# Optimization experiments

Hardware: AMD Instinct MI355X
Metric: run time of the kernel (lower is better)

## Reference

```python
import jax, jax.numpy as jnp
import numpy as np

WIDTH = 2048
NUM_HEADS = 16
HEAD_DIM = WIDTH // NUM_HEADS
WINDOW = 1024
B, T = 4, 2048
MIN_LOGIT = -2.3819763e+38
MAX_WAVELENGTH = 10000.0


def apply_rope(x, positions):
    # x: [b, t, n, h]; RoPE on first half of h, pass-through second half
    b, t, n, h = x.shape
    x_rope, x_pass = jnp.split(x, 2, axis=-1)
    half = x_rope.shape[-1] // 2
    freq_exponents = 2.0 * jnp.arange(half, dtype=jnp.float32) / (2 * half)
    inv_freq = MAX_WAVELENGTH ** (-freq_exponents)  # [half]
    sinusoid = positions.astype(jnp.float32).reshape(1, t, 1, 1) * inv_freq  # [1,t,1,half]
    sin = jnp.sin(sinusoid).astype(x.dtype)
    cos = jnp.cos(sinusoid).astype(x.dtype)
    x1, x2 = jnp.split(x_rope, 2, axis=-1)
    return jnp.concatenate([x1 * cos - x2 * sin, x2 * cos + x1 * sin, x_pass], axis=-1)


def setup_inputs() -> dict:
    key = jax.random.key(0)
    ks = jax.random.split(key, 6)
    x = jax.random.normal(ks[0], (B, T, WIDTH), dtype=jnp.float32)
    segment_pos = jnp.arange(T, dtype=jnp.int32)
    # forward-pass mask: single segment, causal + window
    pos = jnp.arange(T)
    attention_mask = (pos[:, None] >= pos[None, :]) & (pos[:, None] <= pos[None, :] + WINDOW)
    std = np.sqrt(1.0 / WIDTH)
    wq = jax.random.normal(ks[1], (WIDTH, WIDTH), dtype=jnp.float32) * std
    wk = jax.random.normal(ks[2], (HEAD_DIM, WIDTH), dtype=jnp.float32) * std
    wv = jax.random.normal(ks[3], (HEAD_DIM, WIDTH), dtype=jnp.float32) * std
    w_out = jax.random.normal(ks[4], (WIDTH, WIDTH), dtype=jnp.float32) * std
    b_out = jnp.zeros((WIDTH,), dtype=jnp.float32)
    return {"x": x, "segment_pos": segment_pos, "attention_mask": attention_mask,
            "wq": wq, "wk": wk, "wv": wv, "w_out": w_out, "b_out": b_out}


def reference(x, segment_pos, attention_mask, wq, wk, wv, w_out, b_out):
    b, t, _ = x.shape
    q = (x @ wq.T).reshape(b, t, NUM_HEADS, HEAD_DIM)  # [b,t,n,h]
    k = (x @ wk.T).reshape(b, t, 1, HEAD_DIM)          # single shared KV head (MQA)
    v = x @ wv.T                                        # [b,t,h]
    q = apply_rope(q, segment_pos)
    k = apply_rope(k, segment_pos)[:, :, 0]             # [b,t,h]
    logits = jnp.einsum('btnh,bsh->bnts', q, k).astype(jnp.float32) * (HEAD_DIM ** -0.5)
    logits = jnp.where(attention_mask[None, None], logits, MIN_LOGIT)
    probs = jax.nn.softmax(logits, axis=-1).astype(x.dtype)
    encoded = jnp.einsum('bnts,bsh->btnh', probs, v).reshape(b, t, WIDTH)
    return encoded @ w_out.T + b_out
```

## Files before the change

kernel.cpp:

```cpp
#include <hip/hip_runtime.h>
#include <stdint.h>


#define WIDTH_ 2048
#define NHEADS_ 16
#define HD_ 128
#define WINDOW_ 1024
#define B_ 4
#define T_ 2048
#define MROWS_ (B_ * T_)
#define NQKV_ (WIDTH_ + 2 * HD_)

typedef float f32x4 __attribute__((ext_vector_type(4)));
typedef __bf16 bf16x8 __attribute__((ext_vector_type(8)));
typedef float f32x4v __attribute__((ext_vector_type(4)));
typedef unsigned short u16;
typedef unsigned int u32;

__device__ __forceinline__ u16 f2bf(float x) {
  u32 u = __builtin_bit_cast(u32, x);
  return (u16)((u + 0x7FFFu + ((u >> 16) & 1u)) >> 16);
}
__device__ __forceinline__ float bf2f(u16 b) {
  u32 u = ((u32)b) << 16;
  return __builtin_bit_cast(float, u);
}
__device__ __forceinline__ u32 pack2bf(float a, float b) {
  union { __bf16 h[2]; u32 u; } c;
  c.h[0] = (__bf16)a; c.h[1] = (__bf16)b;
  return c.u;
}

__device__ __forceinline__ f32x4 mfma16(bf16x8 a, bf16x8 b, f32x4 c) {
  return __builtin_amdgcn_mfma_f32_16x16x32_bf16(a, b, c, 0, 0, 0);
}

#define GLL16(gp, lp)                                          \
  __builtin_amdgcn_global_load_lds(                            \
      (const __attribute__((address_space(1))) void*)(gp),     \
      (__attribute__((address_space(3))) void*)(lp), 16, 0, 0)

__global__ __launch_bounds__(256) void cvt_f32_bf16(const float* __restrict__ src,
                                                    u16* __restrict__ dst, int n4) {
  int i = blockIdx.x * blockDim.x + threadIdx.x;
  int stride = gridDim.x * blockDim.x;
  for (; i < n4; i += stride) {
    f32x4v v = *reinterpret_cast<const f32x4v*>(src + 4 * (size_t)i);
    u32 lo = (u32)f2bf(v[0]) | ((u32)f2bf(v[1]) << 16);
    u32 hi = (u32)f2bf(v[2]) | ((u32)f2bf(v[3]) << 16);
    uint2 o;
    o.x = lo; o.y = hi;
    *reinterpret_cast<uint2*>(dst + 4 * (size_t)i) = o;
  }
}

__global__ __launch_bounds__(256) void cvt_weights(const float* __restrict__ wq,
                                                   const float* __restrict__ wk,
                                                   const float* __restrict__ wv,
                                                   const float* __restrict__ wo,
                                                   u16* __restrict__ wqkv,
                                                   u16* __restrict__ wob) {
  const int NQ = WIDTH_ * WIDTH_ / 4;
  const int NK = HD_ * WIDTH_ / 4;
  const int NO = WIDTH_ * WIDTH_ / 4;
  const int total = NQ + 2 * NK + NO;
  int i = blockIdx.x * blockDim.x + threadIdx.x;
  int stride = gridDim.x * blockDim.x;
  for (; i < total; i += stride) {
    const float* s;
    u16* d;
    int j;
    if (i < NQ) { s = wq; d = wqkv; j = i; }
    else if (i < NQ + NK) { s = wk; d = wqkv + (size_t)WIDTH_ * WIDTH_; j = i - NQ; }
    else if (i < NQ + 2 * NK) { s = wv; d = wqkv + (size_t)(WIDTH_ + HD_) * WIDTH_; j = i - NQ - NK; }
    else { s = wo; d = wob; j = i - NQ - 2 * NK; }
    f32x4v v = *reinterpret_cast<const f32x4v*>(s + 4 * (size_t)j);
    uint2 o;
    o.x = (u32)f2bf(v[0]) | ((u32)f2bf(v[1]) << 16);
    o.y = (u32)f2bf(v[2]) | ((u32)f2bf(v[3]) << 16);
    *reinterpret_cast<uint2*>(d + 4 * (size_t)j) = o;
  }
}

template <bool F32OUT>
__global__ __launch_bounds__(256) void gemm_bt(const u16* __restrict__ A,
                                               const u16* __restrict__ W,
                                               void* __restrict__ Cout,
                                               const float* __restrict__ bias,
                                               int M, int N, int K) {
  __shared__ alignas(16) u16 As[128 * 32];
  __shared__ alignas(16) u16 Bs[128 * 32];
  const int tid = threadIdx.x;
  const int wid = tid >> 6, lane = tid & 63;
  const int g = lane >> 4, lr = lane & 15;
  const int m0 = blockIdx.y << 7, n0 = blockIdx.x << 7;
  const int wm = wid >> 1, wn = wid & 1;

  const f32x4 vzero = {0.f, 0.f, 0.f, 0.f};
  f32x4 acc[4][4];
#pragma unroll
  for (int i = 0; i < 4; i++)
#pragma unroll
    for (int j = 0; j < 4; j++) acc[i][j] = vzero;

  const int c0 = wid * 2, c1 = wid * 2 + 1;
  const int lrow = lane >> 2;
  const int lcol = (lane & 3) * 8;
  const u16* a0 = A + (size_t)(m0 + c0 * 16 + lrow) * K + lcol;
  const u16* a1 = A + (size_t)(m0 + c1 * 16 + lrow) * K + lcol;
  const u16* b0 = W + (size_t)(n0 + c0 * 16 + lrow) * K + lcol;
  const u16* b1 = W + (size_t)(n0 + c1 * 16 + lrow) * K + lcol;

  for (int k0 = 0; k0 < K; k0 += 32) {
    __syncthreads();
    GLL16(a0 + k0, &As[c0 * 512]);
    GLL16(a1 + k0, &As[c1 * 512]);
    GLL16(b0 + k0, &Bs[c0 * 512]);
    GLL16(b1 + k0, &Bs[c1 * 512]);
    __syncthreads();

    bf16x8 af[4], bfv[4];
#pragma unroll
    for (int mi = 0; mi < 4; mi++)
      af[mi] = *(const bf16x8*)&As[(wm * 64 + mi * 16 + lr) * 32 + g * 8];
#pragma unroll
    for (int ni = 0; ni < 4; ni++)
      bfv[ni] = *(const bf16x8*)&Bs[(wn * 64 + ni * 16 + lr) * 32 + g * 8];
#pragma unroll
    for (int mi = 0; mi < 4; mi++)
#pragma unroll
      for (int ni = 0; ni < 4; ni++)
        acc[mi][ni] = mfma16(af[mi], bfv[ni], acc[mi][ni]);
  }

#pragma unroll
  for (int mi = 0; mi < 4; mi++) {
    int row = m0 + wm * 64 + mi * 16 + g * 4;
#pragma unroll
    for (int ni = 0; ni < 4; ni++) {
      int col = n0 + wn * 64 + ni * 16 + lr;
#pragma unroll
      for (int r = 0; r < 4; r++) {
        float v = acc[mi][ni][r];
        if (F32OUT) {
          ((float*)Cout)[(size_t)(row + r) * N + col] = v + bias[col];
        } else {
          ((u16*)Cout)[(size_t)(row + r) * N + col] = f2bf(v);
        }
      }
    }
  }
}

template <bool F32OUT>
__global__ __launch_bounds__(512, 2) void gemm256(const u16* __restrict__ A,
                                                  const u16* __restrict__ W,
                                                  void* __restrict__ Cout,
                                                  const float* __restrict__ bias,
                                                  int M, int N, int K) {
  __shared__ alignas(16) u16 As[3][256 * 32];
  __shared__ alignas(16) u16 Bs[3][256 * 32];
  const int tid = threadIdx.x;
  const int wid = tid >> 6, lane = tid & 63;
  const int g = lane >> 4, lr = lane & 15;
  const int wm = wid >> 2, wn = wid & 3;

  const int nwg = gridDim.x;
  const int o = blockIdx.x;
  const int wg = (o & 7) * (nwg >> 3) + (o >> 3);
  const int NT = N >> 8;
  const int mt = wg / NT, nt = wg % NT;
  const int m0 = mt << 8, n0 = nt << 8;

  const u16* pa[2];
  const u16* pb[2];
#pragma unroll
  for (int j = 0; j < 2; j++) {
    int row = wid * 32 + j * 16 + (lane >> 2);
    int sc = (lane & 3) ^ ((row >> 1) & 3);
    pa[j] = A + (size_t)(m0 + row) * K + sc * 8;
    pb[j] = W + (size_t)(n0 + row) * K + sc * 8;
  }
  const int ldsoff = wid * 2048;

  const f32x4 vzero = {0.f, 0.f, 0.f, 0.f};
  f32x4 acc[8][4];
#pragma unroll
  for (int i = 0; i < 8; i++)
#pragma unroll
    for (int j = 0; j < 4; j++) acc[i][j] = vzero;

#define STAGE_A(bi, k0)                                        \
  do {                                                         \
    GLL16(pa[0] + (k0), (char*)As[bi] + ldsoff);               \
    GLL16(pa[1] + (k0), (char*)As[bi] + ldsoff + 1024);        \
  } while (0)
#define STAGE_B(bi, k0)                                        \
  do {                                                         \
    GLL16(pb[0] + (k0), (char*)Bs[bi] + ldsoff);               \
    GLL16(pb[1] + (k0), (char*)Bs[bi] + ldsoff + 1024);        \
  } while (0)

  STAGE_A(0, 0); STAGE_B(0, 0);
  STAGE_A(1, 32); STAGE_B(1, 32);
  asm volatile("s_waitcnt vmcnt(4)" ::: "memory");
  __builtin_amdgcn_sched_barrier(0);
  __builtin_amdgcn_s_barrier();

  const int ntk = K >> 5;
  int cur = 0;
  for (int t = 0; t < ntk; ++t) {
    const int nx2 = (cur + 2 >= 3) ? cur - 1 : cur + 2;
    const char* aB = (const char*)As[cur];
    const char* bB = (const char*)Bs[cur];
    const bool pre = (t + 2 < ntk);

    bf16x8 bfv[4], af[4];
#pragma unroll
    for (int ni = 0; ni < 4; ni++) {
      int row = wn * 64 + ni * 16 + lr;
      bfv[ni] = *(const bf16x8*)(bB + row * 64 + ((g ^ ((row >> 1) & 3)) << 4));
    }
#pragma unroll
    for (int mi = 0; mi < 4; mi++) {
      int row = wm * 128 + mi * 16 + lr;
      af[mi] = *(const bf16x8*)(aB + row * 64 + ((g ^ ((row >> 1) & 3)) << 4));
    }
    if (pre) STAGE_A(nx2, (t + 2) << 5);
    __builtin_amdgcn_s_barrier();
    asm volatile("s_waitcnt lgkmcnt(0)" ::: "memory");
    __builtin_amdgcn_sched_barrier(0);
    __builtin_amdgcn_s_setprio(1);
#pragma unroll
    for (int mi = 0; mi < 4; mi++)
#pragma unroll
      for (int ni = 0; ni < 4; ni++)
        acc[mi][ni] = mfma16(af[mi], bfv[ni], acc[mi][ni]);
    __builtin_amdgcn_s_setprio(0);
    __builtin_amdgcn_s_barrier();

    bf16x8 af2[4];
#pragma unroll
    for (int mi = 0; mi < 4; mi++) {
      int row = wm * 128 + 64 + mi * 16 + lr;
      af2[mi] = *(const bf16x8*)(aB + row * 64 + ((g ^ ((row >> 1) & 3)) << 4));
    }
    if (pre) STAGE_B(nx2, (t + 2) << 5);
    __builtin_amdgcn_s_barrier();
    asm volatile("s_waitcnt lgkmcnt(0)" ::: "memory");
    __builtin_amdgcn_sched_barrier(0);
    __builtin_amdgcn_s_setprio(1);
#pragma unroll
    for (int mi = 0; mi < 4; mi++)
#pragma unroll
      for (int ni = 0; ni < 4; ni++)
        acc[mi + 4][ni] = mfma16(af2[mi], bfv[ni], acc[mi + 4][ni]);
    __builtin_amdgcn_s_setprio(0);

    if (pre) {
      asm volatile("s_waitcnt vmcnt(4)" ::: "memory");
    } else if (t + 1 < ntk) {
      asm volatile("s_waitcnt vmcnt(0)" ::: "memory");
    }
    __builtin_amdgcn_sched_barrier(0);
    __builtin_amdgcn_s_barrier();

    cur = (cur + 1 >= 3) ? 0 : cur + 1;
  }
#undef STAGE_A
#undef STAGE_B

#pragma unroll
  for (int mi = 0; mi < 8; mi++) {
    int row = m0 + wm * 128 + mi * 16 + g * 4;
#pragma unroll
    for (int ni = 0; ni < 4; ni++) {
      int col = n0 + wn * 64 + ni * 16 + lr;
#pragma unroll
      for (int r = 0; r < 4; r++) {
        float v = acc[mi][ni][r];
        if (F32OUT) {
          ((float*)Cout)[(size_t)(row + r) * N + col] = v + bias[col];
        } else {
          ((u16*)Cout)[(size_t)(row + r) * N + col] = f2bf(v);
        }
      }
    }
  }
}

__global__ __launch_bounds__(256) void rope_scatter(const u16* __restrict__ Qraw,
                                                    const u16* __restrict__ KVraw,
                                                    const int* __restrict__ segpos,
                                                    u16* __restrict__ Qb,
                                                    u16* __restrict__ Kb,
                                                    u16* __restrict__ VT) {
  const int row = blockIdx.x;
  const int b = row / T_, t = row % T_;
  const float pos = (float)segpos[t];
  const u16* qsrc = Qraw + (size_t)row * WIDTH_;
  const u16* kvsrc = KVraw + (size_t)row * 256;
  const int tid = threadIdx.x;
  const float L2_10K_OVER_32 = 0.4152410118609203f;

  for (int j = tid; j < NHEADS_ * 32; j += 256) {
    int h = j >> 5, d = j & 31;
    float inv = exp2f(-(float)d * L2_10K_OVER_32);
    float ang = pos * inv;
    float sn = sinf(ang), cs = cosf(ang);
    int c1 = h * HD_ + d, c2 = c1 + 32;
    float x1 = bf2f(qsrc[c1]), x2 = bf2f(qsrc[c2]);
    Qb[(size_t)row * WIDTH_ + c1] = f2bf(x1 * cs - x2 * sn);
    Qb[(size_t)row * WIDTH_ + c2] = f2bf(x2 * cs + x1 * sn);
  }
  for (int j = tid; j < NHEADS_ * 64; j += 256) {
    int h = j >> 6, d = j & 63;
    int c = h * HD_ + 64 + d;
    Qb[(size_t)row * WIDTH_ + c] = qsrc[c];
  }
  if (tid < 32) {
    int d = tid;
    float inv = exp2f(-(float)d * L2_10K_OVER_32);
    float ang = pos * inv;
    float sn = sinf(ang), cs = cosf(ang);
    float x1 = bf2f(kvsrc[d]), x2 = bf2f(kvsrc[d + 32]);
    Kb[(size_t)row * HD_ + d] = f2bf(x1 * cs - x2 * sn);
    Kb[(size_t)row * HD_ + d + 32] = f2bf(x2 * cs + x1 * sn);
  } else if (tid >= 64 && tid < 128) {
    int d = tid;
    Kb[(size_t)row * HD_ + d] = kvsrc[d];
  }
  for (int j = tid; j < HD_; j += 256) {
    VT[((size_t)b * HD_ + j) * T_ + t] = kvsrc[HD_ + j];
  }
}

__global__ __launch_bounds__(256, 2) void attn(const u16* __restrict__ Qb,
                                               const u16* __restrict__ Kb,
                                               const u16* __restrict__ VT,
                                               u16* __restrict__ Eb) {
  __shared__ alignas(16) u16 Ks[2][64 * 128];
  __shared__ alignas(16) u16 Vs[2][128 * 64];
  __shared__ alignas(16) u16 Ps[4][2][16 * 64];

  const int tid = threadIdx.x;
  const int wid = tid >> 6, lane = tid & 63;
  const int g = lane >> 4, lr = lane & 15;
  const int nqt = T_ / 128;
  const int qt = blockIdx.x % nqt;
  const int n = (blockIdx.x / nqt) % NHEADS_;
  const int b = blockIdx.x / (nqt * NHEADS_);
  const int q0b = qt * 128;
  const int q0w = q0b + wid * 32;

  const char* kptr = (const char*)(Kb + (size_t)b * T_ * HD_);
  const char* vptr = (const char*)(VT + (size_t)b * HD_ * T_);

  const char* srcb[8];
  int smul;
  if (wid < 2) {
    smul = HD_ * 2;
#pragma unroll
    for (int i = 0; i < 8; i++) {
      int row = wid * 32 + i * 4 + (lane >> 4);
      int c = (lane & 15) << 4;
      srcb[i] = kptr + (size_t)row * 256 + (c ^ ((row & 7) << 4));
    }
  } else {
    smul = 2;
#pragma unroll
    for (int i = 0; i < 8; i++) {
      int row = (wid - 2) * 64 + i * 8 + (lane >> 3);
      int c = (lane & 7) << 4;
      srcb[i] = vptr + (size_t)row * (T_ * 2) + (c ^ ((row & 7) << 4));
    }
  }

  bf16x8 qf[2][4];
#pragma unroll
  for (int su = 0; su < 2; su++) {
    const u16* qrow = Qb + (size_t)(b * T_ + q0w + su * 16 + lr) * WIDTH_ + n * HD_;
#pragma unroll
    for (int kk = 0; kk < 4; kk++) qf[su][kk] = *(const bf16x8*)(qrow + kk * 32 + g * 8);
  }

  const f32x4 vzero = {0.f, 0.f, 0.f, 0.f};
  f32x4 eacc[2][8];
#pragma unroll
  for (int su = 0; su < 2; su++)
#pragma unroll
    for (int i = 0; i < 8; i++) eacc[su][i] = vzero;
  float m_r[2] = {-1e30f, -1e30f}, l_r[2] = {0.f, 0.f};

  const float CSC = 0.08838834764831845f * 1.4426950408889634f;
  const int sbeg = (q0b > WINDOW_) ? (q0b - WINDOW_) : 0;
  const int nt = (q0b + 127 - sbeg) / 64 + 1;

  char* Pw = (char*)Ps[wid];
  const int swz = (lr & 7) << 4;

  auto STAGE = [&](int s0, int buf) {
    char* dbase = (wid < 2) ? ((char*)Ks[buf] + wid * 8192)
                            : ((char*)Vs[buf] + (wid - 2) * 8192);
#pragma unroll
    for (int i = 0; i < 8; i++) {
      GLL16(srcb[i] + (size_t)s0 * smul, dbase + i * 1024);
    }
  };

  STAGE(sbeg, 0);
  __syncthreads();

  for (int t = 0; t < nt; ++t) {
    const int s0 = sbeg + t * 64;
    const int cur = t & 1;
    if (t + 1 < nt) STAGE(s0 + 64, cur ^ 1);

    const bool active = (s0 <= q0w + 31) && (s0 + 63 >= q0w - WINDOW_);
    if (active) {
      const char* kB = (const char*)Ks[cur];
      const char* vB = (const char*)Vs[cur];
      f32x4 sacc[2][4];
#pragma unroll
      for (int su = 0; su < 2; su++)
#pragma unroll
        for (int h = 0; h < 4; h++) sacc[su][h] = vzero;
#pragma unroll
      for (int h = 0; h < 4; h++) {
        bf16x8 kf[4];
        const int krow = h * 16 + lr;
#pragma unroll
        for (int kk = 0; kk < 4; kk++)
          kf[kk] = *(const bf16x8*)(kB + krow * 256 + ((kk * 64 + g * 16) ^ swz));
#pragma unroll
        for (int su = 0; su < 2; su++)
#pragma unroll
          for (int kk = 0; kk < 4; kk++)
            sacc[su][h] = mfma16(kf[kk], qf[su][kk], sacc[su][h]);
      }

      const bool wint = (s0 + 63 <= q0w) && (s0 >= q0w + 31 - WINDOW_);
#pragma unroll
      for (int su = 0; su < 2; su++) {
        const int qq = q0w + su * 16 + lr;
        float pm = -1e30f;
        if (wint) {
#pragma unroll
          for (int h = 0; h < 4; h++)
#pragma unroll
            for (int r = 0; r < 4; r++) {
              float v = sacc[su][h][r] * CSC;
              sacc[su][h][r] = v;
              pm = fmaxf(pm, v);
            }
        } else {
#pragma unroll
          for (int h = 0; h < 4; h++)
#pragma unroll
            for (int r = 0; r < 4; r++) {
              int s = s0 + h * 16 + g * 4 + r;
              bool ok = (s <= qq) && (s + WINDOW_ >= qq);
              float v = ok ? sacc[su][h][r] * CSC : -1e30f;
              sacc[su][h][r] = v;
              pm = fmaxf(pm, v);
            }
        }
        pm = fmaxf(pm, __shfl_xor(pm, 16));
        pm = fmaxf(pm, __shfl_xor(pm, 32));
        if (!__all(pm <= m_r[su] + 8.f)) {
          float mnew = fmaxf(m_r[su], pm);
          float alpha = exp2f(m_r[su] - mnew);
          m_r[su] = mnew;
          l_r[su] *= alpha;
          float aq[4];
#pragma unroll
          for (int r = 0; r < 4; r++) aq[r] = __shfl(alpha, g * 4 + r);
#pragma unroll
          for (int i = 0; i < 8; i++) {
            f32x4 e = eacc[su][i];
#pragma unroll
            for (int r = 0; r < 4; r++) e[r] *= aq[r];
            eacc[su][i] = e;
          }
        }
        float rs = 0.f;
#pragma unroll
        for (int h = 0; h < 4; h++)
#pragma unroll
          for (int r = 0; r < 4; r++) {
            float e = exp2f(sacc[su][h][r] - m_r[su]);
            sacc[su][h][r] = e;
            rs += e;
          }
        rs += __shfl_xor(rs, 16);
        rs += __shfl_xor(rs, 32);
        l_r[su] += rs;

#pragma unroll
        for (int h = 0; h < 4; h++) {
          int base = (lr * 128 + h * 32 + g * 8) ^ swz;
          uint2 w2;
          w2.x = pack2bf(sacc[su][h][0], sacc[su][h][1]);
          w2.y = pack2bf(sacc[su][h][2], sacc[su][h][3]);
          *(uint2*)(Pw + su * 2048 + base) = w2;
        }
      }

      bf16x8 pf[2][2];
#pragma unroll
      for (int su = 0; su < 2; su++) {
        pf[su][0] = *(const bf16x8*)(Pw + su * 2048 + ((lr * 128 + g * 16) ^ swz));
        pf[su][1] = *(const bf16x8*)(Pw + su * 2048 + ((lr * 128 + 64 + g * 16) ^ swz));
      }
#pragma unroll
      for (int ht = 0; ht < 8; ht++) {
        const int vrow = ht * 16 + lr;
        bf16x8 vf0 = *(const bf16x8*)(vB + vrow * 128 + ((g * 16) ^ swz));
        bf16x8 vf1 = *(const bf16x8*)(vB + vrow * 128 + ((64 + g * 16) ^ swz));
#pragma unroll
        for (int su = 0; su < 2; su++) {
          eacc[su][ht] = mfma16(pf[su][0], vf0, eacc[su][ht]);
          eacc[su][ht] = mfma16(pf[su][1], vf1, eacc[su][ht]);
        }
      }
    }
    __syncthreads();
  }

#pragma unroll
  for (int su = 0; su < 2; su++) {
    float lq[4];
#pragma unroll
    for (int r = 0; r < 4; r++) lq[r] = 1.f / __shfl(l_r[su], g * 4 + r);
#pragma unroll
    for (int ht = 0; ht < 8; ht++) {
#pragma unroll
      for (int r = 0; r < 4; r++) {
        int row = b * T_ + q0w + su * 16 + g * 4 + r;
        int col = n * HD_ + ht * 16 + lr;
        Eb[(size_t)row * WIDTH_ + col] = f2bf(eacc[su][ht][r] * lq[r]);
      }
    }
  }
}

extern "C" void kernel_launch(void* const* d_in, const int* in_sizes, int n_in,
                              void* d_out, int out_size, void* d_ws, size_t ws_size,
                              hipStream_t stream) {
  (void)in_sizes; (void)n_in; (void)out_size; (void)ws_size;
  const float* x = (const float*)d_in[0];
  const int* segpos = (const int*)d_in[1];
  const float* wq = (const float*)d_in[3];
  const float* wk = (const float*)d_in[4];
  const float* wv = (const float*)d_in[5];
  const float* w_out = (const float*)d_in[6];
  const float* b_out = (const float*)d_in[7];

  char* p = (char*)d_ws;
  u16* xb = (u16*)p;    p += (size_t)MROWS_ * WIDTH_ * 2;
  u16* wqkv = (u16*)p;  p += (size_t)NQKV_ * WIDTH_ * 2;
  u16* wob = (u16*)p;   p += (size_t)WIDTH_ * WIDTH_ * 2;
  u16* qraw = (u16*)p;  p += (size_t)MROWS_ * WIDTH_ * 2;
  u16* kvraw = (u16*)p; p += (size_t)MROWS_ * 256 * 2;
  u16* qb = (u16*)p;    p += (size_t)MROWS_ * WIDTH_ * 2;
  u16* kb = (u16*)p;    p += (size_t)MROWS_ * HD_ * 2;
  u16* vt = (u16*)p;    p += (size_t)B_ * HD_ * T_ * 2;
  u16* eb = xb;

  cvt_f32_bf16<<<4096, 256, 0, stream>>>(x, xb, MROWS_ * WIDTH_ / 4);
  cvt_weights<<<2048, 256, 0, stream>>>(wq, wk, wv, w_out, wqkv, wob);

  gemm256<false><<<(MROWS_ / 256) * (WIDTH_ / 256), 512, 0, stream>>>(
      xb, wqkv, qraw, nullptr, MROWS_, WIDTH_, WIDTH_);
  gemm_bt<false><<<dim3(256 / 128, MROWS_ / 128), 256, 0, stream>>>(
      xb, wqkv + (size_t)WIDTH_ * WIDTH_, kvraw, nullptr, MROWS_, 256, WIDTH_);

  rope_scatter<<<MROWS_, 256, 0, stream>>>(qraw, kvraw, segpos, qb, kb, vt);
  attn<<<B_ * NHEADS_ * (T_ / 128), 256, 0, stream>>>(qb, kb, vt, eb);

  gemm256<true><<<(MROWS_ / 256) * (WIDTH_ / 256), 512, 0, stream>>>(
      eb, wob, d_out, b_out, MROWS_, WIDTH_, WIDTH_);
}
```

Before: 357.7 us.

## Split attention block into 8 waves of 16 query rows and prescale Q

The attention kernel now runs 512 threads per block, with 8 waves each owning 16 query rows instead of 4 waves with 32 rows. Staging of K/V tiles is spread across all 8 waves. The softmax scale and log2(e) are folded into Q during the RoPE pass, which removes a per-logit multiply. Block-to-query-tile mapping is rotated per batch to balance the uneven window workloads. The aim is more waves to hide latency and fewer per-wave registers, at the cost of each K/V fragment load feeding only one MFMA instead of two, plus extra rounding of Q.

```diff
diff --git a/kernel.cpp b/kernel.cpp
--- a/kernel.cpp
+++ b/kernel.cpp
@@ -39,6 +39,8 @@
   __builtin_amdgcn_global_load_lds(                            \
       (const __attribute__((address_space(1))) void*)(gp),     \
       (__attribute__((address_space(3))) void*)(lp), 16, 0, 0)
+
+#define CSC_ 0.12753101296631838f
 
 __global__ __launch_bounds__(256) void cvt_f32_bf16(const float* __restrict__ src,
                                                     u16* __restrict__ dst, int n4) {
@@ -62,8 +64,7 @@
                                                    u16* __restrict__ wob) {
   const int NQ = WIDTH_ * WIDTH_ / 4;
   const int NK = HD_ * WIDTH_ / 4;
-  const int NO = WIDTH_ * WIDTH_ / 4;
-  const int total = NQ + 2 * NK + NO;
+  const int total = 2 * NQ + 2 * NK;
   int i = blockIdx.x * blockDim.x + threadIdx.x;
   int stride = gridDim.x * blockDim.x;
   for (; i < total; i += stride) {
@@ -310,13 +311,13 @@
     float sn = sinf(ang), cs = cosf(ang);
     int c1 = h * HD_ + d, c2 = c1 + 32;
     float x1 = bf2f(qsrc[c1]), x2 = bf2f(qsrc[c2]);
-    Qb[(size_t)row * WIDTH_ + c1] = f2bf(x1 * cs - x2 * sn);
-    Qb[(size_t)row * WIDTH_ + c2] = f2bf(x2 * cs + x1 * sn);
+    Qb[(size_t)row * WIDTH_ + c1] = f2bf((x1 * cs - x2 * sn) * CSC_);
+    Qb[(size_t)row * WIDTH_ + c2] = f2bf((x2 * cs + x1 * sn) * CSC_);
   }
   for (int j = tid; j < NHEADS_ * 64; j += 256) {
     int h = j >> 6, d = j & 63;
     int c = h * HD_ + 64 + d;
-    Qb[(size_t)row * WIDTH_ + c] = qsrc[c];
+    Qb[(size_t)row * WIDTH_ + c] = f2bf(bf2f(qsrc[c]) * CSC_);
   }
   if (tid < 32) {
     int d = tid;
@@ -335,75 +336,74 @@
   }
 }
 
-__global__ __launch_bounds__(256, 2) void attn(const u16* __restrict__ Qb,
+__global__ __launch_bounds__(512, 4) void attn(const u16* __restrict__ Qb,
                                                const u16* __restrict__ Kb,
                                                const u16* __restrict__ VT,
                                                u16* __restrict__ Eb) {
   __shared__ alignas(16) u16 Ks[2][64 * 128];
   __shared__ alignas(16) u16 Vs[2][128 * 64];
-  __shared__ alignas(16) u16 Ps[4][2][16 * 64];
+  __shared__ alignas(16) u16 Ps[8][16 * 64];
 
   const int tid = threadIdx.x;
   const int wid = tid >> 6, lane = tid & 63;
   const int g = lane >> 4, lr = lane & 15;
-  const int nqt = T_ / 128;
-  const int qt = blockIdx.x % nqt;
-  const int n = (blockIdx.x / nqt) % NHEADS_;
-  const int b = blockIdx.x / (nqt * NHEADS_);
+
+  const int bid = blockIdx.x;
+  const int grp = bid >> 4;
+  const int b = grp >> 4, n = grp & 15;
+  const int qt = ((bid & 15) + b * 4) & 15;
   const int q0b = qt * 128;
-  const int q0w = q0b + wid * 32;
+  const int q0w = q0b + wid * 16;
 
   const char* kptr = (const char*)(Kb + (size_t)b * T_ * HD_);
   const char* vptr = (const char*)(VT + (size_t)b * HD_ * T_);
 
-  const char* srcb[8];
-  int smul;
-  if (wid < 2) {
+  const char* srcb[4];
+  int smul, dst0;
+  if (wid < 4) {
     smul = HD_ * 2;
 #pragma unroll
-    for (int i = 0; i < 8; i++) {
-      int row = wid * 32 + i * 4 + (lane >> 4);
+    for (int i = 0; i < 4; i++) {
+      int row = wid * 16 + i * 4 + (lane >> 4);
       int c = (lane & 15) << 4;
       srcb[i] = kptr + (size_t)row * 256 + (c ^ ((row & 7) << 4));
     }
+    dst0 = wid * 4096;
   } else {
     smul = 2;
 #pragma unroll
-    for (int i = 0; i < 8; i++) {
-      int row = (wid - 2) * 64 + i * 8 + (lane >> 3);
+    for (int i = 0; i < 4; i++) {
+      int row = (wid - 4) * 32 + i * 8 + (lane >> 3);
       int c = (lane & 7) << 4;
       srcb[i] = vptr + (size_t)row * (T_ * 2) + (c ^ ((row & 7) << 4));
     }
-  }
-
-  bf16x8 qf[2][4];
-#pragma unroll
-  for (int su = 0; su < 2; su++) {
-    const u16* qrow = Qb + (size_t)(b * T_ + q0w + su * 16 + lr) * WIDTH_ + n * HD_;
-#pragma unroll
-    for (int kk = 0; kk < 4; kk++) qf[su][kk] = *(const bf16x8*)(qrow + kk * 32 + g * 8);
+    dst0 = (wid - 4) * 4096;
+  }
+
+  bf16x8 qf[4];
+  {
+    const u16* qrow = Qb + (size_t)(b * T_ + q0w + lr) * WIDTH_ + n * HD_;
+#pragma unroll
+    for (int kk = 0; kk < 4; kk++) qf[kk] = *(const bf16x8*)(qrow + kk * 32 + g * 8);
   }
 
   const f32x4 vzero = {0.f, 0.f, 0.f, 0.f};
-  f32x4 eacc[2][8];
-#pragma unroll
-  for (int su = 0; su < 2; su++)
-#pragma unroll
-    for (int i = 0; i < 8; i++) eacc[su][i] = vzero;
-  float m_r[2] = {-1e30f, -1e30f}, l_r[2] = {0.f, 0.f};
-
-  const float CSC = 0.08838834764831845f * 1.4426950408889634f;
+  f32x4 eacc[8];
+#pragma unroll
+  for (int i = 0; i < 8; i++) eacc[i] = vzero;
+  float m_r = -1e30f, l_r = 0.f;
+
   const int sbeg = (q0b > WINDOW_) ? (q0b - WINDOW_) : 0;
   const int nt = (q0b + 127 - sbeg) / 64 + 1;
 
   char* Pw = (char*)Ps[wid];
   const int swz = (lr & 7) << 4;
+  const int q = q0w + lr;
 
   auto STAGE = [&](int s0, int buf) {
-    char* dbase = (wid < 2) ? ((char*)Ks[buf] + wid * 8192)
-                            : ((char*)Vs[buf] + (wid - 2) * 8192);
-#pragma unroll
-    for (int i = 0; i < 8; i++) {
+    char* dbase = (wid < 4) ? ((char*)Ks[buf] + dst0) : ((char*)Vs[buf] + dst0);
+#pragma unroll
+    for (int i = 0; i < 4; i++) {
       GLL16(srcb[i] + (size_t)s0 * smul, dbase + i * 1024);
     }
   };
@@ -416,130 +416,107 @@
     const int cur = t & 1;
     if (t + 1 < nt) STAGE(s0 + 64, cur ^ 1);
 
-    const bool active = (s0 <= q0w + 31) && (s0 + 63 >= q0w - WINDOW_);
+    const bool active = (s0 <= q0w + 15) && (s0 + 63 >= q0w - WINDOW_);
     if (active) {
       const char* kB = (const char*)Ks[cur];
       const char* vB = (const char*)Vs[cur];
-      f32x4 sacc[2][4];
-#pragma unroll
-      for (int su = 0; su < 2; su++)
-#pragma unroll
-        for (int h = 0; h < 4; h++) sacc[su][h] = vzero;
+      f32x4 sacc[4];
+#pragma unroll
+      for (int h = 0; h < 4; h++) sacc[h] = vzero;
 #pragma unroll
       for (int h = 0; h < 4; h++) {
-        bf16x8 kf[4];
         const int krow = h * 16 + lr;
 #pragma unroll
-        for (int kk = 0; kk < 4; kk++)
-          kf[kk] = *(const bf16x8*)(kB + krow * 256 + ((kk * 64 + g * 16) ^ swz));
-#pragma unroll
-        for (int su = 0; su < 2; su++)
-#pragma unroll
-          for (int kk = 0; kk < 4; kk++)
-            sacc[su][h] = mfma16(kf[kk], qf[su][kk], sacc[su][h]);
-      }
-
-      const bool wint = (s0 + 63 <= q0w) && (s0 >= q0w + 31 - WINDOW_);
-#pragma unroll
-      for (int su = 0; su < 2; su++) {
-        const int qq = q0w + su * 16 + lr;
-        float pm = -1e30f;
-        if (wint) {
-#pragma unroll
-          for (int h = 0; h < 4; h++)
-#pragma unroll
-            for (int r = 0; r < 4; r++) {
-              float v = sacc[su][h][r] * CSC;
-              sacc[su][h][r] = v;
-              pm = fmaxf(pm, v);
-            }
-        } else {
-#pragma unroll
-          for (int h = 0; h < 4; h++)
-#pragma unroll
-            for (int r = 0; r < 4; r++) {
-              int s = s0 + h * 16 + g * 4 + r;
-              bool ok = (s <= qq) && (s + WINDOW_ >= qq);
-              float v = ok ? sacc[su][h][r] * CSC : -1e30f;
-              sacc[su][h][r] = v;
-              pm = fmaxf(pm, v);
-            }
+        for (int kk = 0; kk < 4; kk++) {
+          bf16x8 kf = *(const bf16x8*)(kB + krow * 256 + ((kk * 64 + g * 16) ^ swz));
+          sacc[h] = mfma16(kf, qf[kk], sacc[h]);
         }
-        pm = fmaxf(pm, __shfl_xor(pm, 16));
-        pm = fmaxf(pm, __shfl_xor(pm, 32));
-        if (!__all(pm <= m_r[su] + 8.f)) {
-          float mnew = fmaxf(m_r[su], pm);
-          float alpha = exp2f(m_r[su] - mnew);
-          m_r[su] = mnew;
-          l_r[su] *= alpha;
-          float aq[4];
-#pragma unroll
-          for (int r = 0; r < 4; r++) aq[r] = __shfl(alpha, g * 4 + r);
-#pragma unroll
-          for (int i = 0; i < 8; i++) {
-            f32x4 e = eacc[su][i];
-#pragma unroll
-            for (int r = 0; r < 4; r++) e[r] *= aq[r];
-            eacc[su][i] = e;
+      }
+
+      const bool wint = (s0 + 63 <= q0w) && (s0 >= q0w + 15 - WINDOW_);
+      float pm = -1e30f;
+      if (wint) {
+#pragma unroll
+        for (int h = 0; h < 4; h++)
+#pragma unroll
+          for (int r = 0; r < 4; r++) pm = fmaxf(pm, sacc[h][r]);
+      } else {
+#pragma unroll
+        for (int h = 0; h < 4; h++)
+#pragma unroll
+          for (int r = 0; r < 4; r++) {
+            int s = s0 + h * 16 + g * 4 + r;
+            bool ok = (s <= q) && (s + WINDOW_ >= q);
+            float v = ok ? sacc[h][r] : -1e30f;
+            sacc[h][r] = v;
+            pm = fmaxf(pm, v);
           }
+      }
+      pm = fmaxf(pm, __shfl_xor(pm, 16));
+      pm = fmaxf(pm, __shfl_xor(pm, 32));
+
+      if (!__all(pm <= m_r + 8.f)) {
+        float mnew = fmaxf(m_r, pm);
+        float alpha = exp2f(m_r - mnew);
+        m_r = mnew;
+        l_r *= alpha;
+        float aq[4];
+#pragma unroll
+        for (int r = 0; r < 4; r++) aq[r] = __shfl(alpha, g * 4 + r);
+#pragma unroll
+        for (int i = 0; i < 8; i++) {
+          f32x4 e = eacc[i];
+#pragma unroll
+          for (int r = 0; r < 4; r++) e[r] *= aq[r];
+          eacc[i] = e;
         }
-        float rs = 0.f;
-#pragma unroll
-        for (int h = 0; h < 4; h++)
-#pragma unroll
-          for (int r = 0; r < 4; r++) {
-            float e = exp2f(sacc[su][h][r] - m_r[su]);
-            sacc[su][h][r] = e;
-            rs += e;
-          }
-        rs += __shfl_xor(rs, 16);
-        rs += __shfl_xor(rs, 32);
-        l_r[su] += rs;
-
-#pragma unroll
-        for (int h = 0; h < 4; h++) {
-          int base = (lr * 128 + h * 32 + g * 8) ^ swz;
-          uint2 w2;
-          w2.x = pack2bf(sacc[su][h][0], sacc[su][h][1]);
-          w2.y = pack2bf(sacc[su][h][2], sacc[su][h][3]);
-          *(uint2*)(Pw + su * 2048 + base) = w2;
+      }
+      float rs = 0.f;
+#pragma unroll
+      for (int h = 0; h < 4; h++)
+#pragma unroll
+        for (int r = 0; r < 4; r++) {
+          float e = exp2f(sacc[h][r] - m_r);
+          sacc[h][r] = e;
+          rs += e;
         }
-      }
-
-      bf16x8 pf[2][2];
-#pragma unroll
-      for (int su = 0; su < 2; su++) {
-        pf[su][0] = *(const bf16x8*)(Pw + su * 2048 + ((lr * 128 + g * 16) ^ swz));
-        pf[su][1] = *(const bf16x8*)(Pw + su * 2048 + ((lr * 128 + 64 + g * 16) ^ swz));
-      }
+      rs += __shfl_xor(rs, 16);
+      rs += __shfl_xor(rs, 32);
+      l_r += rs;
+
+#pragma unroll
+      for (int h = 0; h < 4; h++) {
+        int base = (lr * 128 + h * 32 + g * 8) ^ swz;
+        uint2 w2;
+        w2.x = pack2bf(sacc[h][0], sacc[h][1]);
+        w2.y = pack2bf(sacc[h][2], sacc[h][3]);
+        *(uint2*)(Pw + base) = w2;
+      }
+      bf16x8 pf0 = *(const bf16x8*)(Pw + ((lr * 128 + g * 16) ^ swz));
+      bf16x8 pf1 = *(const bf16x8*)(Pw + ((lr * 128 + 64 + g * 16) ^ swz));
+
 #pragma unroll
       for (int ht = 0; ht < 8; ht++) {
         const int vrow = ht * 16 + lr;
         bf16x8 vf0 = *(const bf16x8*)(vB + vrow * 128 + ((g * 16) ^ swz));
         bf16x8 vf1 = *(const bf16x8*)(vB + vrow * 128 + ((64 + g * 16) ^ swz));
-#pragma unroll
-        for (int su = 0; su < 2; su++) {
-          eacc[su][ht] = mfma16(pf[su][0], vf0, eacc[su][ht]);
-          eacc[su][ht] = mfma16(pf[su][1], vf1, eacc[su][ht]);
-        }
+        eacc[ht] = mfma16(pf0, vf0, eacc[ht]);
+        eacc[ht] = mfma16(pf1, vf1, eacc[ht]);
       }
     }
     __syncthreads();
   }
 
-#pragma unroll
-  for (int su = 0; su < 2; su++) {
-    float lq[4];
-#pragma unroll
-    for (int r = 0; r < 4; r++) lq[r] = 1.f / __shfl(l_r[su], g * 4 + r);
-#pragma unroll
-    for (int ht = 0; ht < 8; ht++) {
-#pragma unroll
-      for (int r = 0; r < 4; r++) {
-        int row = b * T_ + q0w + su * 16 + g * 4 + r;
-        int col = n * HD_ + ht * 16 + lr;
-        Eb[(size_t)row * WIDTH_ + col] = f2bf(eacc[su][ht][r] * lq[r]);
-      }
+  float lq[4];
+#pragma unroll
+  for (int r = 0; r < 4; r++) lq[r] = 1.f / __shfl(l_r, g * 4 + r);
+#pragma unroll
+  for (int ht = 0; ht < 8; ht++) {
+#pragma unroll
+    for (int r = 0; r < 4; r++) {
+      int row = b * T_ + q0w + g * 4 + r;
+      int col = n * HD_ + ht * 16 + lr;
+      Eb[(size_t)row * WIDTH_ + col] = f2bf(eacc[ht][r] * lq[r]);
     }
   }
 }
@@ -576,7 +553,7 @@
       xb, wqkv + (size_t)WIDTH_ * WIDTH_, kvraw, nullptr, MROWS_, 256, WIDTH_);
 
   rope_scatter<<<MROWS_, 256, 0, stream>>>(qraw, kvraw, segpos, qb, kb, vt);
-  attn<<<B_ * NHEADS_ * (T_ / 128), 256, 0, stream>>>(qb, kb, vt, eb);
+  attn<<<B_ * NHEADS_ * (T_ / 128), 512, 0, stream>>>(qb, kb, vt, eb);
 
   gemm256<true><<<(MROWS_ / 256) * (WIDTH_ / 256), 512, 0, stream>>>(
       eb, wob, d_out, b_out, MROWS_, WIDTH_, WIDTH_);
```

Measured after the change: 341.8 us. 1.05x faster.
